# Kernel optimization log

Hardware: AMD Instinct MI355X
Metric: run time of the kernel (lower is better)

## Reference

```python
import jax, jax.numpy as jnp
import numpy as np
import math

NPASS = 10
B = 16384
IN_DIM = 2048
C = 101
PI = 0.5
SIGMA1 = 1.0            # exp(-0)
SIGMA2 = math.exp(-6.0)
LOG_SQRT_2PI = 0.5 * math.log(2.0 * math.pi)


def setup_inputs() -> dict:
    key = jax.random.key(0)
    ks = jax.random.split(key, 7)
    x = jax.random.normal(ks[0], (B, IN_DIM), jnp.float32)
    weight_mu = jax.random.uniform(ks[1], (C, IN_DIM), jnp.float32, -0.2, 0.2)
    weight_rho = jax.random.uniform(ks[2], (C, IN_DIM), jnp.float32, -5.0, -4.0)
    bias_mu = jax.random.uniform(ks[3], (C,), jnp.float32, -0.2, 0.2)
    bias_rho = jax.random.uniform(ks[4], (C,), jnp.float32, -5.0, -4.0)
    eps_w = jax.random.normal(ks[5], (NPASS, C, IN_DIM), jnp.float32)
    eps_b = jax.random.normal(ks[6], (NPASS, C), jnp.float32)
    return {"x": x, "weight_mu": weight_mu, "weight_rho": weight_rho,
            "bias_mu": bias_mu, "bias_rho": bias_rho,
            "eps_w": eps_w, "eps_b": eps_b, "npass": NPASS}


def _mixture_log_prob(v, axes):
    # log( pi*N(v;0,s1) + (1-pi)*N(v;0,s2) ), summed over param axes (per pass)
    lp1 = -LOG_SQRT_2PI - math.log(SIGMA1) - v * v / (2.0 * SIGMA1 ** 2)
    lp2 = -LOG_SQRT_2PI - math.log(SIGMA2) - v * v / (2.0 * SIGMA2 ** 2)
    return jnp.log(PI * jnp.exp(lp1) + (1.0 - PI) * jnp.exp(lp2)).sum(axes)


def _posterior_log_prob(v, mu, sigma, axes):
    return (-LOG_SQRT_2PI - jnp.log(sigma)
            - (v - mu) ** 2 / (2.0 * sigma ** 2)).sum(axes)


def reference(x, weight_mu, weight_rho, bias_mu, bias_rho, eps_w, eps_b, npass):
    # Reparameterized Gaussian sampling (vectorized over npass)
    sigma_w = jnp.log1p(jnp.exp(weight_rho))        # [C, I]
    sigma_b = jnp.log1p(jnp.exp(bias_rho))          # [C]
    w = weight_mu + sigma_w * eps_w                 # [n, C, I]
    b = bias_mu + sigma_b * eps_b                   # [n, C]

    # outputs[i] = x @ w[i].T + b[i]  -> [n, B, C]
    outputs = jnp.einsum('bi,noi->nbo', x, w) + b[:, None, :]
    pred_mean = outputs.mean(0)                     # [B, C]

    # scale-mixture prior and variational posterior log-probs, per pass
    log_priors = _mixture_log_prob(w, (1, 2)) + _mixture_log_prob(b, (1,))
    log_posts = (_posterior_log_prob(w, weight_mu, sigma_w, (1, 2))
                 + _posterior_log_prob(b, bias_mu, sigma_b, (1,)))
    log_prior = log_priors.mean()
    log_posterior = log_posts.mean()

    p = jax.nn.softmax(outputs, axis=-1)            # [n, B, C]
    # trace(diag(p) - p p^T) = sum(p) - sum(p^2) ; avoids [n,B,C,C] outer products
    aleatoric = (p.sum(-1) - (p * p).sum(-1)).mean(0)   # [B]
    p_bar = p.mean(0)                                   # [B, C]
    # trace((p - p_bar)(p - p_bar)^T) = sum((p - p_bar)^2)
    epistemic = ((p - p_bar) ** 2).sum(-1).mean(0)      # [B]

    return pred_mean, log_prior, log_posterior, aleatoric, epistemic
```

## Files before the change

### kernel.cpp

```cpp
#include <hip/hip_runtime.h>
#include <hip/hip_bf16.h>
#include <math.h>

#define NB    16384
#define KDIM  2048
#define NCLS  101
#define NP    10
#define NTOT  (NP*NCLS)
#define NPAD  1024
#define PM_SIZE (NB*NCLS)
#define CI    (NCLS*KDIM)
#define NBLK_PW ((CI + 255) / 256)
#define PAD_ELEMS ((NPAD - NTOT) * KDIM)
#define NT    32

#define LSQ2PI 0.9189385332046727f
#define HALF_INV_S2SQ 81377.39570642986f

typedef __bf16 bf16x8 __attribute__((ext_vector_type(8)));
typedef float f32x4 __attribute__((ext_vector_type(4)));

__device__ __forceinline__ unsigned short f2bf_bits(float f) {
    union { float f; unsigned u; } v; v.f = f;
    unsigned u = v.u;
    unsigned r = u + 0x7FFFu + ((u >> 16) & 1u);
    return (unsigned short)(r >> 16);
}

__device__ __forceinline__ bf16x8 cvt8(float4 a, float4 b) {
    bf16x8 r;
    r[0] = (__bf16)a.x; r[1] = (__bf16)a.y; r[2] = (__bf16)a.z; r[3] = (__bf16)a.w;
    r[4] = (__bf16)b.x; r[5] = (__bf16)b.y; r[6] = (__bf16)b.z; r[7] = (__bf16)b.w;
    return r;
}

__device__ __forceinline__ float mix_logprob(float v) {
    float q = v * v;
    float lp1 = -LSQ2PI - 0.5f * q;
    float lp2 = -LSQ2PI + 6.0f - HALF_INV_S2SQ * q;
    return __logf(0.5f * __expf(lp1) + 0.5f * __expf(lp2));
}

__global__ void prep_weights(const float* __restrict__ wmu, const float* __restrict__ wrho,
                             const float* __restrict__ eps_w,
                             unsigned short* __restrict__ wB, float* __restrict__ partials) {
    const int t = blockIdx.x * 256 + threadIdx.x;
    if (t < PAD_ELEMS) wB[(size_t)NTOT * KDIM + t] = 0;
    float prior = 0.f, post = 0.f;
    if (t < CI) {
        const float mu = wmu[t];
        const float sigma = log1pf(__expf(wrho[t]));
        const float nls = -__logf(sigma);
        const int c = t / KDIM, i = t & (KDIM - 1);
        #pragma unroll
        for (int n = 0; n < NP; ++n) {
            const float eps = eps_w[(size_t)n * CI + t];
            const float w = fmaf(sigma, eps, mu);
            wB[(size_t)(n * NCLS + c) * KDIM + i] = f2bf_bits(w);
            prior += mix_logprob(w);
            post += nls - LSQ2PI - 0.5f * eps * eps;
        }
    }
    for (int off = 32; off; off >>= 1) {
        prior += __shfl_xor(prior, off);
        post  += __shfl_xor(post, off);
    }
    __shared__ float sp[4], so[4];
    const int wid = threadIdx.x >> 6;
    if ((threadIdx.x & 63) == 0) { sp[wid] = prior; so[wid] = post; }
    __syncthreads();
    if (threadIdx.x == 0) {
        partials[blockIdx.x * 2]     = sp[0] + sp[1] + sp[2] + sp[3];
        partials[blockIdx.x * 2 + 1] = so[0] + so[1] + so[2] + so[3];
    }
}

__global__ void prep_bias(const float* __restrict__ bmu, const float* __restrict__ brho,
                          const float* __restrict__ eps_b, const float* __restrict__ partials,
                          float* __restrict__ biasN, float* __restrict__ out) {
    const int t = threadIdx.x;
    float prior = 0.f, post = 0.f, bv = 0.f;
    if (t < NTOT) {
        const int c = t % NCLS;
        const float sigma = log1pf(__expf(brho[c]));
        const float eps = eps_b[t];
        bv = fmaf(sigma, eps, bmu[c]);
        prior = mix_logprob(bv);
        post = -LSQ2PI - __logf(sigma) - 0.5f * eps * eps;
    }
    biasN[t] = bv;
    if (t < NBLK_PW) { prior += partials[2 * t]; post += partials[2 * t + 1]; }
    for (int off = 32; off; off >>= 1) {
        prior += __shfl_xor(prior, off);
        post  += __shfl_xor(post, off);
    }
    __shared__ float sp[16], so[16];
    const int wid = t >> 6;
    if ((t & 63) == 0) { sp[wid] = prior; so[wid] = post; }
    __syncthreads();
    if (t == 0) {
        float a = 0.f, b = 0.f;
        for (int i = 0; i < 16; ++i) { a += sp[i]; b += so[i]; }
        out[PM_SIZE]     = a * (1.0f / NP);
        out[PM_SIZE + 1] = b * (1.0f / NP);
    }
}

__device__ __forceinline__ void stage_half(const unsigned short* __restrict__ G,
                                           int grow0, int k0, int lds_byte_base,
                                           int tid, char* ldsp) {
    #pragma unroll
    for (int l = 0; l < 2; ++l) {
        const int flat = l * 512 + tid;
        const int row = flat >> 3, j = flat & 7;
        const int jsw = j ^ (row & 7);
        const unsigned short* src = G + (size_t)(grow0 + row) * KDIM + k0 + jsw * 8;
        __builtin_amdgcn_global_load_lds(
            (const __attribute__((address_space(1))) void*)src,
            (__attribute__((address_space(3))) void*)(ldsp + lds_byte_base + flat * 16),
            16, 0, 0);
    }
}

#define STAGE_B2(buf, tt) do { \
    stage_half(Bm, bn,       (tt) * 64, 32768 + (buf) * 32768,         tid, ldsp); \
    stage_half(Bm, bn + 128, (tt) * 64, 32768 + (buf) * 32768 + 16384, tid, ldsp); \
} while (0)

#define A_LOAD(SET, tt) do { \
    const float* p_ = X + (size_t)(bm + arow) * KDIM + (tt) * 64 + acol; \
    SET[0] = *(const float4*)p_;        SET[1] = *(const float4*)(p_ + 4); \
    SET[2] = *(const float4*)(p_ + 8);  SET[3] = *(const float4*)(p_ + 12); \
} while (0)

#define A_WRITE(SET, dstbuf) do { \
    char* base_ = ldsp + (dstbuf) * 16384; \
    *(bf16x8*)(base_ + aw0) = cvt8(SET[0], SET[1]); \
    *(bf16x8*)(base_ + aw1) = cvt8(SET[2], SET[3]); \
} while (0)

#define LDA(mf, buf) do { \
    const int row_ = wr * 64 + (mf) * 16 + l15; \
    const char* p_ = ldsp + (buf) * 16384 + row_ * 128; \
    const int sw_ = (row_ & 7) << 4; \
    af[mf][0] = *(const bf16x8*)(p_ + ((l4 << 4) ^ sw_)); \
    af[mf][1] = *(const bf16x8*)(p_ + (((4 + l4) << 4) ^ sw_)); \
} while (0)

#define LDB(nf, buf) do { \
    const int row_ = (wc & 1) * 64 + (nf) * 16 + l15; \
    const char* p_ = ldsp + 32768 + (buf) * 32768 + (wc >> 1) * 16384 + row_ * 128; \
    const int sw_ = (row_ & 7) << 4; \
    bf[nf][0] = *(const bf16x8*)(p_ + ((l4 << 4) ^ sw_)); \
    bf[nf][1] = *(const bf16x8*)(p_ + (((4 + l4) << 4) ^ sw_)); \
} while (0)

#define MM(mp, np) do { \
    __builtin_amdgcn_s_setprio(1); \
    _Pragma("unroll") \
    for (int mi = 0; mi < 2; ++mi) \
        _Pragma("unroll") \
        for (int ni = 0; ni < 2; ++ni) \
            _Pragma("unroll") \
            for (int kk = 0; kk < 2; ++kk) \
                acc[(mp) * 2 + mi][(np) * 2 + ni] = __builtin_amdgcn_mfma_f32_16x16x32_bf16( \
                    af[(mp) * 2 + mi][kk], bf[(np) * 2 + ni][kk], acc[(mp) * 2 + mi][(np) * 2 + ni], 0, 0, 0); \
    __builtin_amdgcn_s_setprio(0); \
} while (0)

#define SBAR() do { \
    __builtin_amdgcn_sched_barrier(0); \
    __builtin_amdgcn_s_barrier(); \
    __builtin_amdgcn_sched_barrier(0); \
} while (0)

#define TILE(t, buf, LSET, WSET) do { \
     \
    LDA(0, buf); LDA(1, buf); \
    LDB(0, buf); LDB(1, buf); \
    if ((t) < NT - 2) { A_LOAD(LSET, (t) + 2); } \
    SBAR(); \
    MM(0, 0); \
    SBAR(); \
     \
    LDB(2, buf); LDB(3, buf); \
    SBAR(); \
    MM(0, 1); \
    SBAR(); \
     \
    LDA(2, buf); LDA(3, buf); \
    __builtin_amdgcn_sched_barrier(0); \
    if ((t) < NT - 2)        { asm volatile("s_waitcnt vmcnt(8)"); } \
    else if ((t) == NT - 2)  { asm volatile("s_waitcnt vmcnt(4)"); } \
    __builtin_amdgcn_sched_barrier(0); \
    if ((t) < NT - 1) { A_WRITE(WSET, (buf) ^ 1); } \
    if ((t) < NT - 2) { STAGE_B2(buf, (t) + 2); } \
    SBAR(); \
    MM(1, 1); \
    MM(1, 0); \
    __builtin_amdgcn_sched_barrier(0); \
    if ((t) < NT - 2)        { asm volatile("s_waitcnt vmcnt(8) lgkmcnt(0)"); __builtin_amdgcn_s_barrier(); } \
    else if ((t) == NT - 2)  { asm volatile("s_waitcnt vmcnt(0) lgkmcnt(0)"); __builtin_amdgcn_s_barrier(); } \
    __builtin_amdgcn_sched_barrier(0); \
} while (0)

__global__ void __launch_bounds__(512, 2) gemm8(
    const float* __restrict__ X,
    const unsigned short* __restrict__ Bm,
    const float* __restrict__ biasN,
    float* __restrict__ Cout)
{
    __shared__ __align__(16) unsigned short lds[49152];
    char* ldsp = (char*)lds;
    const int tid = threadIdx.x;
    const int lane = tid & 63, wid = tid >> 6;
    const int wr = wid >> 2, wc = wid & 3;
    const int l15 = lane & 15, l4 = lane >> 4;

    const int b = blockIdx.x;
    const int wg = (b & 7) * 64 + (b >> 3);
    const int bm = (wg >> 2) * 128;
    const int bn = (wg & 3) * 256;

    const int arow = tid >> 2;
    const int acol = (tid & 3) * 16;
    const int j0 = (2 * tid) & 7, j1 = j0 + 1;
    const int aw0 = arow * 128 + ((j0 ^ (arow & 7)) << 4);
    const int aw1 = arow * 128 + ((j1 ^ (arow & 7)) << 4);

    f32x4 acc[4][4] = {{}};
    bf16x8 af[4][2], bf[4][2];
    float4 aR0[4], aR1[4];

    A_LOAD(aR0, 0);
    STAGE_B2(0, 0);
    A_LOAD(aR1, 1);
    STAGE_B2(1, 1);
    __builtin_amdgcn_sched_barrier(0);
    asm volatile("s_waitcnt vmcnt(12)");
    __builtin_amdgcn_sched_barrier(0);
    A_WRITE(aR0, 0);
    __builtin_amdgcn_sched_barrier(0);
    asm volatile("s_waitcnt vmcnt(8) lgkmcnt(0)");
    __builtin_amdgcn_s_barrier();
    __builtin_amdgcn_sched_barrier(0);

    #pragma unroll 1
    for (int tt = 0; tt < NT / 2; ++tt) {
        const int t0 = 2 * tt;
        TILE(t0,     0, aR0, aR1);
        TILE(t0 + 1, 1, aR1, aR0);
    }

    #pragma unroll
    for (int n = 0; n < 4; ++n) {
        const int col = bn + wc * 64 + n * 16 + l15;
        const float bv = biasN[col];
        #pragma unroll
        for (int m = 0; m < 4; ++m) {
            const int row0 = bm + wr * 64 + m * 16 + l4 * 4;
            #pragma unroll
            for (int r = 0; r < 4; ++r)
                Cout[(size_t)(row0 + r) * NPAD + col] = acc[m][n][r] + bv;
        }
    }
}

__global__ void stats_kernel(const float* __restrict__ Cout, float* __restrict__ out) {
    const int lane = threadIdx.x & 63;
    const int wid = threadIdx.x >> 6;
    const int b = blockIdx.x * 4 + wid;
    const float* row = Cout + (size_t)b * NPAD;
    float* pm = out;
    float* aleat_out = out + PM_SIZE + 2;
    float* epi_out   = out + PM_SIZE + 2 + NB;

    const bool has2 = lane < (NCLS - 64);
    float p1s[NP], p2s[NP];
    float pm1 = 0.f, pm2 = 0.f, pb1 = 0.f, pb2 = 0.f, aleat = 0.f;

    for (int n = 0; n < NP; ++n) {
        const float v1 = row[n * NCLS + lane];
        const float v2 = has2 ? row[n * NCLS + 64 + lane] : -INFINITY;
        float mx = fmaxf(v1, v2);
        for (int off = 32; off; off >>= 1) mx = fmaxf(mx, __shfl_xor(mx, off));
        const float e1 = __expf(v1 - mx);
        const float e2 = has2 ? __expf(v2 - mx) : 0.f;
        float s = e1 + e2;
        for (int off = 32; off; off >>= 1) s += __shfl_xor(s, off);
        const float p1 = e1 / s, p2 = e2 / s;
        float spp = p1 + p2, sq = p1 * p1 + p2 * p2;
        for (int off = 32; off; off >>= 1) {
            spp += __shfl_xor(spp, off);
            sq  += __shfl_xor(sq, off);
        }
        aleat += spp - sq;
        pm1 += v1; pm2 += v2;
        pb1 += p1; pb2 += p2;
        p1s[n] = p1; p2s[n] = p2;
    }
    const float inv_n = 1.0f / NP;
    pb1 *= inv_n; pb2 *= inv_n;
    pm[(size_t)b * NCLS + lane] = pm1 * inv_n;
    if (has2) pm[(size_t)b * NCLS + 64 + lane] = pm2 * inv_n;
    float epi = 0.f;
    #pragma unroll
    for (int n = 0; n < NP; ++n) {
        const float d1 = p1s[n] - pb1;
        const float d2 = p2s[n] - pb2;
        epi += d1 * d1 + d2 * d2;
    }
    for (int off = 32; off; off >>= 1) epi += __shfl_xor(epi, off);
    if (lane == 0) {
        aleat_out[b] = aleat * inv_n;
        epi_out[b]   = epi * inv_n;
    }
}

extern "C" void kernel_launch(void* const* d_in, const int* in_sizes, int n_in,
                              void* d_out, int out_size, void* d_ws, size_t ws_size,
                              hipStream_t stream) {
    const float* x     = (const float*)d_in[0];
    const float* wmu   = (const float*)d_in[1];
    const float* wrho  = (const float*)d_in[2];
    const float* bmu   = (const float*)d_in[3];
    const float* brho  = (const float*)d_in[4];
    const float* eps_w = (const float*)d_in[5];
    const float* eps_b = (const float*)d_in[6];
    float* out = (float*)d_out;

    char* ws = (char*)d_ws;
    const size_t OFF_WB    = 0;
    const size_t OFF_COUT  = OFF_WB + 4194304;
    const size_t OFF_BIASN = OFF_COUT + 67108864;
    const size_t OFF_PART  = OFF_BIASN + 4096;

    unsigned short* wB   = (unsigned short*)(ws + OFF_WB);
    float* Cout     = (float*)(ws + OFF_COUT);
    float* biasN    = (float*)(ws + OFF_BIASN);
    float* partials = (float*)(ws + OFF_PART);

    prep_weights<<<NBLK_PW, 256, 0, stream>>>(wmu, wrho, eps_w, wB, partials);
    prep_bias<<<1, 1024, 0, stream>>>(bmu, brho, eps_b, partials, biasN, out);
    gemm8<<<512, 512, 0, stream>>>(x, wB, biasN, Cout);
    stats_kernel<<<NB / 4, 256, 0, stream>>>(Cout, out);
}
```

Measured before the change: 145.0 us.

## Enlarge GEMM tile, store logits as bf16, merge bias prep into other kernels

The GEMM moves from 128x256 to 256x256 block tiles with a simpler double-buffered pipeline: 128 KB of LDS, 8x4 accumulators per wave and a full wait plus barrier on every k-step. The intermediate logits are now written as bf16 instead of fp32, which halves the write and re-read traffic between the GEMM and the stats kernel. The bias-prep kernel is removed: bias sampling becomes an extra block of prep_weights, and the final prior/posterior reduction moves into stats_kernel, saving one launch. The costs are reduced logit precision before the softmax, higher register pressure, and half as many workgroups (256) to spread across the CUs.

```diff
diff --git a/kernel.cpp b/kernel.cpp
--- a/kernel.cpp
+++ b/kernel.cpp
@@ -27,6 +27,11 @@
     return (unsigned short)(r >> 16);
 }
 
+__device__ __forceinline__ float bfu(unsigned short u) {
+    union { unsigned u; float f; } v; v.u = ((unsigned)u) << 16;
+    return v.f;
+}
+
 __device__ __forceinline__ bf16x8 cvt8(float4 a, float4 b) {
     bf16x8 r;
     r[0] = (__bf16)a.x; r[1] = (__bf16)a.y; r[2] = (__bf16)a.z; r[3] = (__bf16)a.w;
@@ -43,22 +48,42 @@
 
 __global__ void prep_weights(const float* __restrict__ wmu, const float* __restrict__ wrho,
                              const float* __restrict__ eps_w,
-                             unsigned short* __restrict__ wB, float* __restrict__ partials) {
-    const int t = blockIdx.x * 256 + threadIdx.x;
-    if (t < PAD_ELEMS) wB[(size_t)NTOT * KDIM + t] = 0;
+                             const float* __restrict__ bmu, const float* __restrict__ brho,
+                             const float* __restrict__ eps_b,
+                             unsigned short* __restrict__ wB, float* __restrict__ biasN,
+                             float* __restrict__ partials) {
     float prior = 0.f, post = 0.f;
-    if (t < CI) {
-        const float mu = wmu[t];
-        const float sigma = log1pf(__expf(wrho[t]));
-        const float nls = -__logf(sigma);
-        const int c = t / KDIM, i = t & (KDIM - 1);
+    if (blockIdx.x == NBLK_PW) {
         #pragma unroll
-        for (int n = 0; n < NP; ++n) {
-            const float eps = eps_w[(size_t)n * CI + t];
-            const float w = fmaf(sigma, eps, mu);
-            wB[(size_t)(n * NCLS + c) * KDIM + i] = f2bf_bits(w);
-            prior += mix_logprob(w);
-            post += nls - LSQ2PI - 0.5f * eps * eps;
+        for (int q = 0; q < 4; ++q) {
+            const int i = q * 256 + threadIdx.x;
+            float bv = 0.f;
+            if (i < NTOT) {
+                const int c = i % NCLS;
+                const float sigma = log1pf(__expf(brho[c]));
+                const float eps = eps_b[i];
+                bv = fmaf(sigma, eps, bmu[c]);
+                prior += mix_logprob(bv);
+                post += -LSQ2PI - __logf(sigma) - 0.5f * eps * eps;
+            }
+            biasN[i] = bv;
+        }
+    } else {
+        const int t = blockIdx.x * 256 + threadIdx.x;
+        if (t < PAD_ELEMS) wB[(size_t)NTOT * KDIM + t] = 0;
+        if (t < CI) {
+            const float mu = wmu[t];
+            const float sigma = log1pf(__expf(wrho[t]));
+            const float nls = -__logf(sigma);
+            const int c = t / KDIM, i = t & (KDIM - 1);
+            #pragma unroll
+            for (int n = 0; n < NP; ++n) {
+                const float eps = eps_w[(size_t)n * CI + t];
+                const float w = fmaf(sigma, eps, mu);
+                wB[(size_t)(n * NCLS + c) * KDIM + i] = f2bf_bits(w);
+                prior += mix_logprob(w);
+                post += nls - LSQ2PI - 0.5f * eps * eps;
+            }
         }
     }
     for (int off = 32; off; off >>= 1) {
@@ -75,181 +100,112 @@
     }
 }
 
-__global__ void prep_bias(const float* __restrict__ bmu, const float* __restrict__ brho,
-                          const float* __restrict__ eps_b, const float* __restrict__ partials,
-                          float* __restrict__ biasN, float* __restrict__ out) {
-    const int t = threadIdx.x;
-    float prior = 0.f, post = 0.f, bv = 0.f;
-    if (t < NTOT) {
-        const int c = t % NCLS;
-        const float sigma = log1pf(__expf(brho[c]));
-        const float eps = eps_b[t];
-        bv = fmaf(sigma, eps, bmu[c]);
-        prior = mix_logprob(bv);
-        post = -LSQ2PI - __logf(sigma) - 0.5f * eps * eps;
-    }
-    biasN[t] = bv;
-    if (t < NBLK_PW) { prior += partials[2 * t]; post += partials[2 * t + 1]; }
-    for (int off = 32; off; off >>= 1) {
-        prior += __shfl_xor(prior, off);
-        post  += __shfl_xor(post, off);
-    }
-    __shared__ float sp[16], so[16];
-    const int wid = t >> 6;
-    if ((t & 63) == 0) { sp[wid] = prior; so[wid] = post; }
-    __syncthreads();
-    if (t == 0) {
-        float a = 0.f, b = 0.f;
-        for (int i = 0; i < 16; ++i) { a += sp[i]; b += so[i]; }
-        out[PM_SIZE]     = a * (1.0f / NP);
-        out[PM_SIZE + 1] = b * (1.0f / NP);
-    }
-}
-
-__device__ __forceinline__ void stage_half(const unsigned short* __restrict__ G,
-                                           int grow0, int k0, int lds_byte_base,
-                                           int tid, char* ldsp) {
-    #pragma unroll
-    for (int l = 0; l < 2; ++l) {
-        const int flat = l * 512 + tid;
-        const int row = flat >> 3, j = flat & 7;
-        const int jsw = j ^ (row & 7);
-        const unsigned short* src = G + (size_t)(grow0 + row) * KDIM + k0 + jsw * 8;
-        __builtin_amdgcn_global_load_lds(
-            (const __attribute__((address_space(1))) void*)src,
-            (__attribute__((address_space(3))) void*)(ldsp + lds_byte_base + flat * 16),
-            16, 0, 0);
-    }
-}
-
-#define STAGE_B2(buf, tt) do { \
-    stage_half(Bm, bn,       (tt) * 64, 32768 + (buf) * 32768,         tid, ldsp); \
-    stage_half(Bm, bn + 128, (tt) * 64, 32768 + (buf) * 32768 + 16384, tid, ldsp); \
-} while (0)
-
-#define A_LOAD(SET, tt) do { \
-    const float* p_ = X + (size_t)(bm + arow) * KDIM + (tt) * 64 + acol; \
-    SET[0] = *(const float4*)p_;        SET[1] = *(const float4*)(p_ + 4); \
-    SET[2] = *(const float4*)(p_ + 8);  SET[3] = *(const float4*)(p_ + 12); \
-} while (0)
-
-#define A_WRITE(SET, dstbuf) do { \
-    char* base_ = ldsp + (dstbuf) * 16384; \
-    *(bf16x8*)(base_ + aw0) = cvt8(SET[0], SET[1]); \
-    *(bf16x8*)(base_ + aw1) = cvt8(SET[2], SET[3]); \
-} while (0)
-
-#define LDA(mf, buf) do { \
-    const int row_ = wr * 64 + (mf) * 16 + l15; \
-    const char* p_ = ldsp + (buf) * 16384 + row_ * 128; \
-    const int sw_ = (row_ & 7) << 4; \
-    af[mf][0] = *(const bf16x8*)(p_ + ((l4 << 4) ^ sw_)); \
-    af[mf][1] = *(const bf16x8*)(p_ + (((4 + l4) << 4) ^ sw_)); \
-} while (0)
-
-#define LDB(nf, buf) do { \
-    const int row_ = (wc & 1) * 64 + (nf) * 16 + l15; \
-    const char* p_ = ldsp + 32768 + (buf) * 32768 + (wc >> 1) * 16384 + row_ * 128; \
-    const int sw_ = (row_ & 7) << 4; \
-    bf[nf][0] = *(const bf16x8*)(p_ + ((l4 << 4) ^ sw_)); \
-    bf[nf][1] = *(const bf16x8*)(p_ + (((4 + l4) << 4) ^ sw_)); \
-} while (0)
-
-#define MM(mp, np) do { \
-    __builtin_amdgcn_s_setprio(1); \
-    _Pragma("unroll") \
-    for (int mi = 0; mi < 2; ++mi) \
-        _Pragma("unroll") \
-        for (int ni = 0; ni < 2; ++ni) \
-            _Pragma("unroll") \
-            for (int kk = 0; kk < 2; ++kk) \
-                acc[(mp) * 2 + mi][(np) * 2 + ni] = __builtin_amdgcn_mfma_f32_16x16x32_bf16( \
-                    af[(mp) * 2 + mi][kk], bf[(np) * 2 + ni][kk], acc[(mp) * 2 + mi][(np) * 2 + ni], 0, 0, 0); \
-    __builtin_amdgcn_s_setprio(0); \
-} while (0)
-
-#define SBAR() do { \
-    __builtin_amdgcn_sched_barrier(0); \
-    __builtin_amdgcn_s_barrier(); \
-    __builtin_amdgcn_sched_barrier(0); \
-} while (0)
-
-#define TILE(t, buf, LSET, WSET) do { \
-     \
-    LDA(0, buf); LDA(1, buf); \
-    LDB(0, buf); LDB(1, buf); \
-    if ((t) < NT - 2) { A_LOAD(LSET, (t) + 2); } \
-    SBAR(); \
-    MM(0, 0); \
-    SBAR(); \
-     \
-    LDB(2, buf); LDB(3, buf); \
-    SBAR(); \
-    MM(0, 1); \
-    SBAR(); \
-     \
-    LDA(2, buf); LDA(3, buf); \
-    __builtin_amdgcn_sched_barrier(0); \
-    if ((t) < NT - 2)        { asm volatile("s_waitcnt vmcnt(8)"); } \
-    else if ((t) == NT - 2)  { asm volatile("s_waitcnt vmcnt(4)"); } \
-    __builtin_amdgcn_sched_barrier(0); \
-    if ((t) < NT - 1) { A_WRITE(WSET, (buf) ^ 1); } \
-    if ((t) < NT - 2) { STAGE_B2(buf, (t) + 2); } \
-    SBAR(); \
-    MM(1, 1); \
-    MM(1, 0); \
-    __builtin_amdgcn_sched_barrier(0); \
-    if ((t) < NT - 2)        { asm volatile("s_waitcnt vmcnt(8) lgkmcnt(0)"); __builtin_amdgcn_s_barrier(); } \
-    else if ((t) == NT - 2)  { asm volatile("s_waitcnt vmcnt(0) lgkmcnt(0)"); __builtin_amdgcn_s_barrier(); } \
-    __builtin_amdgcn_sched_barrier(0); \
-} while (0)
-
-__global__ void __launch_bounds__(512, 2) gemm8(
+__global__ void __launch_bounds__(512, 2) gemmF(
     const float* __restrict__ X,
     const unsigned short* __restrict__ Bm,
     const float* __restrict__ biasN,
-    float* __restrict__ Cout)
+    unsigned short* __restrict__ Co)
 {
-    __shared__ __align__(16) unsigned short lds[49152];
-    char* ldsp = (char*)lds;
+    __shared__ __align__(16) char ldsp[131072];
     const int tid = threadIdx.x;
     const int lane = tid & 63, wid = tid >> 6;
     const int wr = wid >> 2, wc = wid & 3;
     const int l15 = lane & 15, l4 = lane >> 4;
 
     const int b = blockIdx.x;
-    const int wg = (b & 7) * 64 + (b >> 3);
-    const int bm = (wg >> 2) * 128;
+    const int wg = (b & 7) * 32 + (b >> 3);
+    const int bm = (wg >> 2) * 256;
     const int bn = (wg & 3) * 256;
 
-    const int arow = tid >> 2;
-    const int acol = (tid & 3) * 16;
-    const int j0 = (2 * tid) & 7, j1 = j0 + 1;
-    const int aw0 = arow * 128 + ((j0 ^ (arow & 7)) << 4);
-    const int aw1 = arow * 128 + ((j1 ^ (arow & 7)) << 4);
-
-    f32x4 acc[4][4] = {{}};
-    bf16x8 af[4][2], bf[4][2];
-    float4 aR0[4], aR1[4];
-
-    A_LOAD(aR0, 0);
-    STAGE_B2(0, 0);
-    A_LOAD(aR1, 1);
-    STAGE_B2(1, 1);
+    const int arow = tid >> 1;
+    const int acol = (tid & 1) * 32;
+    const int aj0 = (tid & 1) * 4;
+    int aw[4];
+    #pragma unroll
+    for (int q = 0; q < 4; ++q)
+        aw[q] = arow * 128 + (((aj0 + q) ^ (arow & 7)) << 4);
+
+    f32x4 acc[8][4] = {{}};
+    bf16x8 af[8], bfr[4];
+    float4 aR[8];
+
+#define A_LOADM(tt) do { \
+    const float4* p4_ = (const float4*)(X + (size_t)(bm + arow) * KDIM + (tt) * 64 + acol); \
+    _Pragma("unroll") for (int i_ = 0; i_ < 8; ++i_) aR[i_] = p4_[i_]; \
+} while (0)
+
+#define A_WRITEM(dstbuf) do { \
+    char* base_ = ldsp + (dstbuf) * 32768; \
+    *(bf16x8*)(base_ + aw[0]) = cvt8(aR[0], aR[1]); \
+    *(bf16x8*)(base_ + aw[1]) = cvt8(aR[2], aR[3]); \
+    *(bf16x8*)(base_ + aw[2]) = cvt8(aR[4], aR[5]); \
+    *(bf16x8*)(base_ + aw[3]) = cvt8(aR[6], aR[7]); \
+} while (0)
+
+#define STAGE_B(dstbuf, tt) do { \
+    _Pragma("unroll") for (int l_ = 0; l_ < 4; ++l_) { \
+        const int flat_ = l_ * 512 + tid;               \
+        const int row_ = flat_ >> 3, j_ = flat_ & 7; \
+        const int jsw_ = j_ ^ (row_ & 7); \
+        const unsigned short* src_ = Bm + (size_t)(bn + row_) * KDIM + (tt) * 64 + jsw_ * 8; \
+        __builtin_amdgcn_global_load_lds( \
+            (const __attribute__((address_space(1))) void*)src_, \
+            (__attribute__((address_space(3))) void*)(ldsp + 65536 + (dstbuf) * 32768 + flat_ * 16), \
+            16, 0, 0); \
+    } \
+} while (0)
+
+#define LDALL(kk, buf) do { \
+    _Pragma("unroll") for (int mf_ = 0; mf_ < 8; ++mf_) { \
+        const int row_ = wr * 128 + mf_ * 16 + l15; \
+        af[mf_] = *(const bf16x8*)(ldsp + (buf) * 32768 + row_ * 128 + ((((kk) * 4 + l4) ^ (row_ & 7)) << 4)); \
+    } \
+    _Pragma("unroll") for (int nf_ = 0; nf_ < 4; ++nf_) { \
+        const int row_ = wc * 64 + nf_ * 16 + l15; \
+        bfr[nf_] = *(const bf16x8*)(ldsp + 65536 + (buf) * 32768 + row_ * 128 + ((((kk) * 4 + l4) ^ (row_ & 7)) << 4)); \
+    } \
+} while (0)
+
+#define MMH() do { \
+    __builtin_amdgcn_s_setprio(1); \
+    _Pragma("unroll") for (int mf_ = 0; mf_ < 8; ++mf_) \
+        _Pragma("unroll") for (int nf_ = 0; nf_ < 4; ++nf_) \
+            acc[mf_][nf_] = __builtin_amdgcn_mfma_f32_16x16x32_bf16(af[mf_], bfr[nf_], acc[mf_][nf_], 0, 0, 0); \
+    __builtin_amdgcn_s_setprio(0); \
+} while (0)
+
+#define TILE(t, buf) do { \
+    const bool more_ = (t) + 1 < NT; \
+    if (more_) { A_LOADM((t) + 1); STAGE_B((buf) ^ 1, (t) + 1); } \
+    __builtin_amdgcn_sched_barrier(0); \
+    LDALL(0, buf); \
+    MMH(); \
+    LDALL(1, buf); \
+    MMH(); \
+    __builtin_amdgcn_sched_barrier(0); \
+    if (more_) { \
+        A_WRITEM((buf) ^ 1);                        \
+        __builtin_amdgcn_sched_barrier(0); \
+        asm volatile("s_waitcnt vmcnt(0) lgkmcnt(0)"); \
+        __builtin_amdgcn_sched_barrier(0); \
+        __builtin_amdgcn_s_barrier(); \
+        __builtin_amdgcn_sched_barrier(0); \
+    } \
+} while (0)
+
+    A_LOADM(0);
+    STAGE_B(0, 0);
+    A_WRITEM(0);
     __builtin_amdgcn_sched_barrier(0);
-    asm volatile("s_waitcnt vmcnt(12)");
-    __builtin_amdgcn_sched_barrier(0);
-    A_WRITE(aR0, 0);
-    __builtin_amdgcn_sched_barrier(0);
-    asm volatile("s_waitcnt vmcnt(8) lgkmcnt(0)");
+    asm volatile("s_waitcnt vmcnt(0) lgkmcnt(0)");
     __builtin_amdgcn_s_barrier();
     __builtin_amdgcn_sched_barrier(0);
 
     #pragma unroll 1
     for (int tt = 0; tt < NT / 2; ++tt) {
         const int t0 = 2 * tt;
-        TILE(t0,     0, aR0, aR1);
-        TILE(t0 + 1, 1, aR1, aR0);
+        TILE(t0, 0);
+        TILE(t0 + 1, 1);
     }
 
     #pragma unroll
@@ -257,20 +213,22 @@
         const int col = bn + wc * 64 + n * 16 + l15;
         const float bv = biasN[col];
         #pragma unroll
-        for (int m = 0; m < 4; ++m) {
-            const int row0 = bm + wr * 64 + m * 16 + l4 * 4;
+        for (int m = 0; m < 8; ++m) {
+            const int row0 = bm + wr * 128 + m * 16 + l4 * 4;
             #pragma unroll
             for (int r = 0; r < 4; ++r)
-                Cout[(size_t)(row0 + r) * NPAD + col] = acc[m][n][r] + bv;
-        }
-    }
-}
-
-__global__ void stats_kernel(const float* __restrict__ Cout, float* __restrict__ out) {
+                Co[(size_t)(row0 + r) * NPAD + col] = f2bf_bits(acc[m][n][r] + bv);
+        }
+    }
+}
+
+__global__ void stats_kernel(const unsigned short* __restrict__ Co,
+                             const float* __restrict__ partials,
+                             float* __restrict__ out) {
     const int lane = threadIdx.x & 63;
     const int wid = threadIdx.x >> 6;
     const int b = blockIdx.x * 4 + wid;
-    const float* row = Cout + (size_t)b * NPAD;
+    const unsigned short* row = Co + (size_t)b * NPAD;
     float* pm = out;
     float* aleat_out = out + PM_SIZE + 2;
     float* epi_out   = out + PM_SIZE + 2 + NB;
@@ -280,8 +238,8 @@
     float pm1 = 0.f, pm2 = 0.f, pb1 = 0.f, pb2 = 0.f, aleat = 0.f;
 
     for (int n = 0; n < NP; ++n) {
-        const float v1 = row[n * NCLS + lane];
-        const float v2 = has2 ? row[n * NCLS + 64 + lane] : -INFINITY;
+        const float v1 = bfu(row[n * NCLS + lane]);
+        const float v2 = has2 ? bfu(row[n * NCLS + 64 + lane]) : -INFINITY;
         float mx = fmaxf(v1, v2);
         for (int off = 32; off; off >>= 1) mx = fmaxf(mx, __shfl_xor(mx, off));
         const float e1 = __expf(v1 - mx);
@@ -315,6 +273,21 @@
         aleat_out[b] = aleat * inv_n;
         epi_out[b]   = epi * inv_n;
     }
+    if (blockIdx.x == 0 && wid == 0) {
+        float a = 0.f, c = 0.f;
+        for (int i = lane; i < NBLK_PW + 1; i += 64) {
+            a += partials[2 * i];
+            c += partials[2 * i + 1];
+        }
+        for (int off = 32; off; off >>= 1) {
+            a += __shfl_xor(a, off);
+            c += __shfl_xor(c, off);
+        }
+        if (lane == 0) {
+            out[PM_SIZE]     = a * (1.0f / NP);
+            out[PM_SIZE + 1] = c * (1.0f / NP);
+        }
+    }
 }
 
 extern "C" void kernel_launch(void* const* d_in, const int* in_sizes, int n_in,
@@ -332,16 +305,16 @@
     char* ws = (char*)d_ws;
     const size_t OFF_WB    = 0;
     const size_t OFF_COUT  = OFF_WB + 4194304;
-    const size_t OFF_BIASN = OFF_COUT + 67108864;
+    const size_t OFF_BIASN = OFF_COUT + 33554432;
     const size_t OFF_PART  = OFF_BIASN + 4096;
 
     unsigned short* wB   = (unsigned short*)(ws + OFF_WB);
-    float* Cout     = (float*)(ws + OFF_COUT);
+    unsigned short* Co   = (unsigned short*)(ws + OFF_COUT);
     float* biasN    = (float*)(ws + OFF_BIASN);
     float* partials = (float*)(ws + OFF_PART);
 
-    prep_weights<<<NBLK_PW, 256, 0, stream>>>(wmu, wrho, eps_w, wB, partials);
-    prep_bias<<<1, 1024, 0, stream>>>(bmu, brho, eps_b, partials, biasN, out);
-    gemm8<<<512, 512, 0, stream>>>(x, wB, biasN, Cout);
-    stats_kernel<<<NB / 4, 256, 0, stream>>>(Cout, out);
-}
+    prep_weights<<<NBLK_PW + 1, 256, 0, stream>>>(wmu, wrho, eps_w, bmu, brho, eps_b,
+                                                  wB, biasN, partials);
+    gemmF<<<256, 512, 0, stream>>>(x, wB, biasN, Co);
+    stats_kernel<<<NB / 4, 256, 0, stream>>>(Co, partials, out);
+}
```

Result: slower. 210.0 us (+44.8%).
